# Kernel tuning notes

Measured on AMD Instinct MI355X. Metric: run time of the kernel, lower is better.

Reference implementation:

```python
import jax, jax.numpy as jnp
import numpy as np

B, S, D, H = 2, 2048, 1024, 16
DK = D // H


def setup_inputs() -> dict:
    key = jax.random.key(0)
    ks = jax.random.split(key, 8)
    Q = jax.random.normal(ks[0], (B, S, D), dtype=jnp.float32)
    K = jax.random.normal(ks[1], (B, S, D), dtype=jnp.float32)
    V = jax.random.normal(ks[2], (B, S, D), dtype=jnp.float32)
    scale = 0.02
    W_q = jax.random.normal(ks[3], (D, D), dtype=jnp.float32) * scale
    W_k = jax.random.normal(ks[4], (D, D), dtype=jnp.float32) * scale
    W_v = jax.random.normal(ks[5], (D, D), dtype=jnp.float32) * scale
    W_o = jax.random.normal(ks[6], (D, D), dtype=jnp.float32) * scale
    b_q = jnp.zeros((D,), jnp.float32)
    b_k = jnp.zeros((D,), jnp.float32)
    b_v = jnp.zeros((D,), jnp.float32)
    b_o = jnp.zeros((D,), jnp.float32)
    # causal mask, broadcastable [1,1,S,S]; mask==0 positions are masked out
    mask = jnp.tril(jnp.ones((S, S), jnp.int32))[None, None, :, :]
    return dict(Q=Q, K=K, V=V, W_q=W_q, b_q=b_q, W_k=W_k, b_k=b_k,
                W_v=W_v, b_v=b_v, W_o=W_o, b_o=b_o, mask=mask)


def reference(Q, K, V, W_q, b_q, W_k, b_k, W_v, b_v, W_o, b_o, mask):
    # linear projections (torch Linear equivalent up to weight layout)
    q = Q @ W_q + b_q   # [B,S,D]
    k = K @ W_k + b_k
    v = V @ W_v + b_v
    # split heads -> [B,H,S,DK]
    q = q.reshape(B, S, H, DK).transpose(0, 2, 1, 3)
    k = k.reshape(B, S, H, DK).transpose(0, 2, 1, 3)
    v = v.reshape(B, S, H, DK).transpose(0, 2, 1, 3)
    # scaled dot-product attention with explicit [B,H,S,S] scores
    scores = jnp.einsum('bhqd,bhkd->bhqk', q, k) / jnp.sqrt(jnp.float32(DK))
    scores = jnp.where(mask == 0, jnp.float32(-1e9), scores)
    attn = jax.nn.softmax(scores, axis=-1)
    out = jnp.einsum('bhqk,bhkd->bhqd', attn, v)
    # merge heads and output projection
    out = out.transpose(0, 2, 1, 3).reshape(B, S, D)
    return out @ W_o + b_o
```

## Files before the change

### kernel.cpp

```cpp
#include <hip/hip_runtime.h>


typedef unsigned short u16;
typedef __attribute__((ext_vector_type(8))) short s8v;
typedef __attribute__((ext_vector_type(4))) float f4v;

#define S_ 2048
#define D_ 1024
#define H_ 16
#define DK_ 64

__device__ __forceinline__ u16 f2bf(float f) {
  unsigned u = __builtin_bit_cast(unsigned, f);
  u += 0x7fffu + ((u >> 16) & 1u);
  return (u16)(u >> 16);
}
__device__ __forceinline__ u16 f2bf_t(float f) {
  return (u16)(__builtin_bit_cast(unsigned, f) >> 16);
}

__device__ __forceinline__ void gld_lds16(const u16* g, u16* l) {
  __builtin_amdgcn_global_load_lds(
      (const __attribute__((address_space(1))) unsigned int*)g,
      (__attribute__((address_space(3))) unsigned int*)l, 16, 0, 0);
}

__global__ __launch_bounds__(256) void prep(
    const float* __restrict__ Q, const float* __restrict__ K, const float* __restrict__ V,
    u16* __restrict__ Qc, u16* __restrict__ Kc, u16* __restrict__ Vc,
    const float* __restrict__ W0, const float* __restrict__ W1,
    const float* __restrict__ W2, const float* __restrict__ W3,
    u16* __restrict__ T0, u16* __restrict__ T1, u16* __restrict__ T2, u16* __restrict__ T3) {
  int bid = blockIdx.x, tid = threadIdx.x;
  if (bid < 3072) {
    int z = bid >> 10, t = bid & 1023;
    const float* s = z == 0 ? Q : z == 1 ? K : V;
    u16*         d = z == 0 ? Qc : z == 1 ? Kc : Vc;
    const int n4 = (2 * S_ * D_) / 4;
    for (int idx = t * 256 + tid; idx < n4; idx += 1024 * 256) {
      float4 f = ((const float4*)s)[idx];
      unsigned lo = (unsigned)f2bf(f.x) | ((unsigned)f2bf(f.y) << 16);
      unsigned hi = (unsigned)f2bf(f.z) | ((unsigned)f2bf(f.w) << 16);
      ((uint2*)d)[idx] = make_uint2(lo, hi);
    }
  } else {
    int wb = bid - 3072;
    int z = wb >> 10, t = wb & 1023;
    const float* W = z == 0 ? W0 : z == 1 ? W1 : z == 2 ? W2 : W3;
    u16*         T = z == 0 ? T0 : z == 1 ? T1 : z == 2 ? T2 : T3;
    __shared__ float tile[32][33];
    int tx = tid & 31, ty = tid >> 5;
    int c0 = (t & 31) * 32, r0 = (t >> 5) * 32;
#pragma unroll
    for (int i = 0; i < 32; i += 8)
      tile[ty + i][tx] = W[(size_t)(r0 + ty + i) * D_ + c0 + tx];
    __syncthreads();
#pragma unroll
    for (int i = 0; i < 32; i += 8)
      T[(size_t)(c0 + ty + i) * D_ + r0 + tx] = f2bf(tile[tx][ty + i]);
  }
}

#define BM_ 128
#define BK_ 64

template <int NJ, int MODE>
__device__ __forceinline__ void gemm_core(const u16* __restrict__ A, const u16* __restrict__ Bt,
                                          const float* __restrict__ bias, void* __restrict__ out,
                                          float oscale, u16* lds) {
  constexpr int BN = NJ * 32;
  u16* Al = lds;
  u16* Bl = lds + BM_ * BK_;
  int tid = threadIdx.x;
  int w = tid >> 6, lane = tid & 63, quad = lane >> 4, col = lane & 15;
  int wm = (w >> 1) * 64, wn = (w & 1) * (NJ * 16);
  int m0 = blockIdx.y * BM_, n0 = blockIdx.x * BN;
  f4v acc[4][NJ] = {};
  const u16* Ag = A + (size_t)m0 * 1024;
  const u16* Bg = Bt + (size_t)n0 * 1024;
  int sr = tid >> 3, ss = tid & 7;

  for (int k0 = 0; k0 < 1024; k0 += BK_) {
    __syncthreads();
#pragma unroll
    for (int c = 0; c < 4; ++c) {
      int r = c * 32 + sr;
      int gs = ss ^ (r & 7);
      gld_lds16(Ag + (size_t)r * 1024 + k0 + gs * 8, &Al[r * BK_ + ss * 8]);
    }
#pragma unroll
    for (int c = 0; c < BN / 32; ++c) {
      int r = c * 32 + sr;
      int gs = ss ^ (r & 7);
      gld_lds16(Bg + (size_t)r * 1024 + k0 + gs * 8, &Bl[r * BK_ + ss * 8]);
    }
    __syncthreads();
#pragma unroll
    for (int hf = 0; hf < 2; ++hf) {
      s8v af[4], bfr[NJ];
#pragma unroll
      for (int i = 0; i < 4; ++i) {
        int row = wm + i * 16 + col;
        int sl = (hf * 4 + quad) ^ (row & 7);
        af[i] = *(const s8v*)&Al[row * BK_ + sl * 8];
      }
#pragma unroll
      for (int j = 0; j < NJ; ++j) {
        int row = wn + j * 16 + col;
        int sl = (hf * 4 + quad) ^ (row & 7);
        bfr[j] = *(const s8v*)&Bl[row * BK_ + sl * 8];
      }
#pragma unroll
      for (int i = 0; i < 4; ++i)
#pragma unroll
        for (int j = 0; j < NJ; ++j)
          acc[i][j] = __builtin_amdgcn_mfma_f32_16x16x32_bf16(af[i], bfr[j], acc[i][j], 0, 0, 0);
    }
  }

  if (MODE == 1) {
    __syncthreads();
    u16* scr = lds + w * 2304;
    int h = (n0 + wn) >> 6;
    int dkl = lane & 31, sh = (lane >> 5) * 32;
    int mg0 = m0 + wm + sh;
    int bb = mg0 >> 11, s0g = mg0 & 2047;
    u16* ob = (u16*)out + ((size_t)(bb * H_ + h) * DK_) * S_;
#pragma unroll
    for (int t = 0; t < 2; ++t) {
#pragma unroll
      for (int j2 = 2 * t; j2 < 2 * t + 2; ++j2) {
        float bv = bias[n0 + wn + j2 * 16 + col];
        int rloc = j2 * 16 + col - t * 32;
#pragma unroll
        for (int i = 0; i < 4; ++i)
#pragma unroll
          for (int r = 0; r < 4; ++r)
            scr[rloc * 72 + i * 16 + quad * 4 + r] = f2bf(acc[i][j2][r] + bv);
      }
      __builtin_amdgcn_wave_barrier();
      u16* op = ob + (size_t)(t * 32 + dkl) * S_ + s0g;
#pragma unroll
      for (int c = 0; c < 4; ++c)
        *(uint4*)&op[c * 8] = *(const uint4*)&scr[dkl * 72 + sh + c * 8];
      __builtin_amdgcn_wave_barrier();
    }
    return;
  }

#pragma unroll
  for (int i = 0; i < 4; ++i) {
#pragma unroll
    for (int j = 0; j < NJ; ++j) {
      int n = n0 + wn + j * 16 + col;
      float bb = bias[n];
#pragma unroll
      for (int r = 0; r < 4; ++r) {
        int m = m0 + wm + i * 16 + quad * 4 + r;
        float v = (acc[i][j][r] + bb) * oscale;
        if (MODE == 2) {
          ((float*)out)[(size_t)m * 1024 + n] = v;
        } else {
          int b = m >> 11, s = m & 2047, h = n >> 6, dk = n & 63;
          ((u16*)out)[((size_t)(b * H_ + h) * S_ + s) * DK_ + dk] = f2bf(v);
        }
      }
    }
  }
}

#define CEXPQ 0.18033688f

__global__ __launch_bounds__(256) void gemm_qkv(
    const u16* __restrict__ A0, const u16* __restrict__ A1, const u16* __restrict__ A2,
    const u16* __restrict__ B0, const u16* __restrict__ B1, const u16* __restrict__ B2,
    const float* __restrict__ bi0, const float* __restrict__ bi1, const float* __restrict__ bi2,
    u16* __restrict__ o0, u16* __restrict__ o1, u16* __restrict__ o2) {
  __shared__ __attribute__((aligned(16))) u16 lds[BM_ * BK_ + 128 * BK_];
  int z = blockIdx.z;
  const u16* A = z == 0 ? A0 : z == 1 ? A1 : A2;
  const u16* Bt = z == 0 ? B0 : z == 1 ? B1 : B2;
  const float* bias = z == 0 ? bi0 : z == 1 ? bi1 : bi2;
  u16* o = z == 0 ? o0 : z == 1 ? o1 : o2;
  if (z == 2)
    gemm_core<4, 1>(A, Bt, bias, o, 1.0f, lds);
  else
    gemm_core<4, 0>(A, Bt, bias, o, z == 0 ? CEXPQ : 1.0f, lds);
}

__global__ __launch_bounds__(256, 5) void gemm_out(const u16* __restrict__ A, const u16* __restrict__ Bt,
                                                   const float* __restrict__ bias, float* __restrict__ out) {
  __shared__ __attribute__((aligned(16))) u16 lds[BM_ * BK_ + 64 * BK_];
  gemm_core<2, 2>(A, Bt, bias, out, 1.0f, lds);
}

#define KT_ 64
#define PSTR 72

__global__ __launch_bounds__(256) void attn_fused(const u16* __restrict__ qb, const u16* __restrict__ kb,
                                                  const u16* __restrict__ vtb, u16* __restrict__ ao) {
  __shared__ __attribute__((aligned(16))) u16 Kt[KT_ * PSTR];
  __shared__ __attribute__((aligned(16))) u16 Vts[DK_ * PSTR];
  __shared__ __attribute__((aligned(16))) u16 Pl[4][16 * PSTR];
  int bh = blockIdx.y, b = bh >> 4, h = bh & 15;
  int j = blockIdx.x;
  int lo_base = j * 64, hi_base = (31 - j) * 64;
  int tid = threadIdx.x, w = tid >> 6, lane = tid & 63, quad = lane >> 4, col = lane & 15;
  const u16* Qh = qb + (size_t)bh * S_ * DK_;
  const u16* Kh = kb + (size_t)bh * S_ * DK_;
  const u16* Vh = vtb + (size_t)bh * DK_ * S_;
  int krow = tid >> 3, kcol = (tid & 7) * 8;

  int lo_qmin = lo_base + w * 16, hi_qmin = hi_base + w * 16;
  s8v qlo0 = *(const s8v*)(Qh + (size_t)(lo_qmin + col) * DK_ + quad * 8);
  s8v qlo1 = *(const s8v*)(Qh + (size_t)(lo_qmin + col) * DK_ + 32 + quad * 8);
  s8v qhi0 = *(const s8v*)(Qh + (size_t)(hi_qmin + col) * DK_ + quad * 8);
  s8v qhi1 = *(const s8v*)(Qh + (size_t)(hi_qmin + col) * DK_ + 32 + quad * 8);

  f4v Olo[4] = {}, Ohi[4] = {};
  float lslo[4] = {}, lshi[4] = {};

  int nk = hi_base + 64;
  uint4 k0r = *(const uint4*)(Kh + (size_t)krow * DK_ + kcol);
  uint4 k1r = *(const uint4*)(Kh + (size_t)(32 + krow) * DK_ + kcol);
  uint4 v0r = *(const uint4*)(Vh + (size_t)krow * S_ + kcol);
  uint4 v1r = *(const uint4*)(Vh + (size_t)(32 + krow) * S_ + kcol);

  for (int kt = 0; kt < nk; kt += KT_) {
    __syncthreads();
    *(uint4*)&Kt[krow * PSTR + kcol] = k0r;
    *(uint4*)&Kt[(32 + krow) * PSTR + kcol] = k1r;
    *(uint4*)&Vts[krow * PSTR + kcol] = v0r;
    *(uint4*)&Vts[(32 + krow) * PSTR + kcol] = v1r;
    __syncthreads();
    int kn = kt + KT_;
    if (kn < nk) {
      k0r = *(const uint4*)(Kh + (size_t)(kn + krow) * DK_ + kcol);
      k1r = *(const uint4*)(Kh + (size_t)(kn + 32 + krow) * DK_ + kcol);
      v0r = *(const uint4*)(Vh + (size_t)krow * S_ + kn + kcol);
      v1r = *(const uint4*)(Vh + (size_t)(32 + krow) * S_ + kn + kcol);
    }

    s8v kf[4][2], vf[4][2];
#pragma unroll
    for (int ks = 0; ks < 4; ++ks) {
      kf[ks][0] = *(const s8v*)&Kt[(ks * 16 + col) * PSTR + quad * 8];
      kf[ks][1] = *(const s8v*)&Kt[(ks * 16 + col) * PSTR + 32 + quad * 8];
    }
#pragma unroll
    for (int d = 0; d < 4; ++d) {
      vf[d][0] = *(const s8v*)&Vts[(d * 16 + col) * PSTR + quad * 8];
      vf[d][1] = *(const s8v*)&Vts[(d * 16 + col) * PSTR + 32 + quad * 8];
    }

    auto process = [&](const s8v& q0, const s8v& q1, int qmin, f4v* O, float* ls) {
      f4v sc[4];
#pragma unroll
      for (int ks = 0; ks < 4; ++ks) {
        f4v t = {0.f, 0.f, 0.f, 0.f};
        t = __builtin_amdgcn_mfma_f32_16x16x32_bf16(q0, kf[ks][0], t, 0, 0, 0);
        t = __builtin_amdgcn_mfma_f32_16x16x32_bf16(q1, kf[ks][1], t, 0, 0, 0);
        sc[ks] = t;
      }
      bool full = (kt + KT_ - 1 <= qmin);
#pragma unroll
      for (int r = 0; r < 4; ++r) {
        float p0, p1, p2, p3;
        if (full) {
          p0 = exp2f(sc[0][r]);
          p1 = exp2f(sc[1][r]);
          p2 = exp2f(sc[2][r]);
          p3 = exp2f(sc[3][r]);
        } else {
          int qr = qmin + quad * 4 + r;
          p0 = (kt + col)      <= qr ? exp2f(sc[0][r]) : 0.f;
          p1 = (kt + 16 + col) <= qr ? exp2f(sc[1][r]) : 0.f;
          p2 = (kt + 32 + col) <= qr ? exp2f(sc[2][r]) : 0.f;
          p3 = (kt + 48 + col) <= qr ? exp2f(sc[3][r]) : 0.f;
        }
        ls[r] += (p0 + p1) + (p2 + p3);
        int row = quad * 4 + r;
        Pl[w][row * PSTR + col]      = f2bf_t(p0);
        Pl[w][row * PSTR + 16 + col] = f2bf_t(p1);
        Pl[w][row * PSTR + 32 + col] = f2bf_t(p2);
        Pl[w][row * PSTR + 48 + col] = f2bf_t(p3);
      }
      __builtin_amdgcn_wave_barrier();
      s8v pa0 = *(const s8v*)&Pl[w][col * PSTR + quad * 8];
      s8v pa1 = *(const s8v*)&Pl[w][col * PSTR + 32 + quad * 8];
#pragma unroll
      for (int d = 0; d < 4; ++d) {
        O[d] = __builtin_amdgcn_mfma_f32_16x16x32_bf16(pa0, vf[d][0], O[d], 0, 0, 0);
        O[d] = __builtin_amdgcn_mfma_f32_16x16x32_bf16(pa1, vf[d][1], O[d], 0, 0, 0);
      }
      __builtin_amdgcn_wave_barrier();
    };

    process(qhi0, qhi1, hi_qmin, Ohi, lshi);
    if (kt <= lo_qmin + 15)
      process(qlo0, qlo1, lo_qmin, Olo, lslo);
  }

#pragma unroll
  for (int g = 0; g < 2; ++g) {
    f4v* O = g ? Olo : Ohi;
    float* ls = g ? lslo : lshi;
    int qmin = g ? lo_qmin : hi_qmin;
#pragma unroll
    for (int r = 0; r < 4; ++r) {
      float l = ls[r];
      l += __shfl_xor(l, 1);
      l += __shfl_xor(l, 2);
      l += __shfl_xor(l, 4);
      l += __shfl_xor(l, 8);
      float inv = 1.0f / l;
      size_t row = (size_t)(b * S_ + qmin + quad * 4 + r);
#pragma unroll
      for (int d = 0; d < 4; ++d)
        ao[row * D_ + h * DK_ + d * 16 + col] = f2bf(O[d][r] * inv);
    }
  }
}

extern "C" void kernel_launch(void* const* d_in, const int* in_sizes, int n_in,
                              void* d_out, int out_size, void* d_ws, size_t ws_size,
                              hipStream_t stream) {
  const float* Q  = (const float*)d_in[0];
  const float* K  = (const float*)d_in[1];
  const float* V  = (const float*)d_in[2];
  const float* Wq = (const float*)d_in[3];
  const float* bq = (const float*)d_in[4];
  const float* Wk = (const float*)d_in[5];
  const float* bk = (const float*)d_in[6];
  const float* Wv = (const float*)d_in[7];
  const float* bv = (const float*)d_in[8];
  const float* Wo = (const float*)d_in[9];
  const float* bo = (const float*)d_in[10];

  char* p = (char*)d_ws;
  const size_t TEN = (size_t)2 * S_ * D_ * 2;
  const size_t WT  = (size_t)D_ * D_ * 2;
  u16* Qc  = (u16*)p; p += TEN;
  u16* Kc  = (u16*)p; p += TEN;
  u16* Vc  = (u16*)p; p += TEN;
  u16* Wqt = (u16*)p; p += WT;
  u16* Wkt = (u16*)p; p += WT;
  u16* Wvt = (u16*)p; p += WT;
  u16* Wot = (u16*)p; p += WT;
  u16* qb  = (u16*)p; p += TEN;
  u16* kbf = (u16*)p; p += TEN;
  u16* vtb = (u16*)p; p += TEN;
  u16* ao  = (u16*)p; p += TEN;

  prep<<<7168, 256, 0, stream>>>(Q, K, V, Qc, Kc, Vc, Wq, Wk, Wv, Wo, Wqt, Wkt, Wvt, Wot);
  gemm_qkv<<<dim3(D_ / 128, 32, 3), 256, 0, stream>>>(Qc, Kc, Vc, Wqt, Wkt, Wvt, bq, bk, bv, qb, kbf, vtb);
  attn_fused<<<dim3(16, 2 * H_), 256, 0, stream>>>(qb, kbf, vtb, ao);
  gemm_out<<<dim3(D_ / 64, 32), 256, 0, stream>>>(ao, Wot, bo, (float*)d_out);
}
```

Before: 243.4 us.

## Split attention hi/lo query tiles across 8 waves and shrink output GEMM tile

The attention kernel moves from 256 threads, where each wave handles both a high and a low query tile, to 512 threads where waves 0-3 take the high tile and waves 4-7 the low tile. K/V staging is spread over all threads, and low-tile waves skip compute once past their causal range. This doubles the waves per block to raise latency hiding and parallelism over a 512-block grid. The output GEMM is templated to a 64x64 tile with a doubled grid so more blocks are available. The cost is load imbalance between the two wave groups and more per-block tile overhead in the smaller GEMM.

```diff
diff --git a/kernel.cpp b/kernel.cpp
--- a/kernel.cpp
+++ b/kernel.cpp
@@ -61,21 +61,21 @@
   }
 }
 
-#define BM_ 128
 #define BK_ 64
 
-template <int NJ, int MODE>
+template <int MI, int NJ, int MODE>
 __device__ __forceinline__ void gemm_core(const u16* __restrict__ A, const u16* __restrict__ Bt,
                                           const float* __restrict__ bias, void* __restrict__ out,
                                           float oscale, u16* lds) {
+  constexpr int BM = MI * 32;
   constexpr int BN = NJ * 32;
   u16* Al = lds;
-  u16* Bl = lds + BM_ * BK_;
+  u16* Bl = lds + BM * BK_;
   int tid = threadIdx.x;
   int w = tid >> 6, lane = tid & 63, quad = lane >> 4, col = lane & 15;
-  int wm = (w >> 1) * 64, wn = (w & 1) * (NJ * 16);
-  int m0 = blockIdx.y * BM_, n0 = blockIdx.x * BN;
-  f4v acc[4][NJ] = {};
+  int wm = (w >> 1) * (MI * 16), wn = (w & 1) * (NJ * 16);
+  int m0 = blockIdx.y * BM, n0 = blockIdx.x * BN;
+  f4v acc[MI][NJ] = {};
   const u16* Ag = A + (size_t)m0 * 1024;
   const u16* Bg = Bt + (size_t)n0 * 1024;
   int sr = tid >> 3, ss = tid & 7;
@@ -83,7 +83,7 @@
   for (int k0 = 0; k0 < 1024; k0 += BK_) {
     __syncthreads();
 #pragma unroll
-    for (int c = 0; c < 4; ++c) {
+    for (int c = 0; c < BM / 32; ++c) {
       int r = c * 32 + sr;
       int gs = ss ^ (r & 7);
       gld_lds16(Ag + (size_t)r * 1024 + k0 + gs * 8, &Al[r * BK_ + ss * 8]);
@@ -97,9 +97,9 @@
     __syncthreads();
 #pragma unroll
     for (int hf = 0; hf < 2; ++hf) {
-      s8v af[4], bfr[NJ];
-#pragma unroll
-      for (int i = 0; i < 4; ++i) {
+      s8v af[MI], bfr[NJ];
+#pragma unroll
+      for (int i = 0; i < MI; ++i) {
         int row = wm + i * 16 + col;
         int sl = (hf * 4 + quad) ^ (row & 7);
         af[i] = *(const s8v*)&Al[row * BK_ + sl * 8];
@@ -111,7 +111,7 @@
         bfr[j] = *(const s8v*)&Bl[row * BK_ + sl * 8];
       }
 #pragma unroll
-      for (int i = 0; i < 4; ++i)
+      for (int i = 0; i < MI; ++i)
 #pragma unroll
         for (int j = 0; j < NJ; ++j)
           acc[i][j] = __builtin_amdgcn_mfma_f32_16x16x32_bf16(af[i], bfr[j], acc[i][j], 0, 0, 0);
@@ -133,7 +133,7 @@
         float bv = bias[n0 + wn + j2 * 16 + col];
         int rloc = j2 * 16 + col - t * 32;
 #pragma unroll
-        for (int i = 0; i < 4; ++i)
+        for (int i = 0; i < MI; ++i)
 #pragma unroll
           for (int r = 0; r < 4; ++r)
             scr[rloc * 72 + i * 16 + quad * 4 + r] = f2bf(acc[i][j2][r] + bv);
@@ -149,7 +149,7 @@
   }
 
 #pragma unroll
-  for (int i = 0; i < 4; ++i) {
+  for (int i = 0; i < MI; ++i) {
 #pragma unroll
     for (int j = 0; j < NJ; ++j) {
       int n = n0 + wn + j * 16 + col;
@@ -176,149 +176,132 @@
     const u16* __restrict__ B0, const u16* __restrict__ B1, const u16* __restrict__ B2,
     const float* __restrict__ bi0, const float* __restrict__ bi1, const float* __restrict__ bi2,
     u16* __restrict__ o0, u16* __restrict__ o1, u16* __restrict__ o2) {
-  __shared__ __attribute__((aligned(16))) u16 lds[BM_ * BK_ + 128 * BK_];
+  __shared__ __attribute__((aligned(16))) u16 lds[128 * BK_ + 128 * BK_];
   int z = blockIdx.z;
   const u16* A = z == 0 ? A0 : z == 1 ? A1 : A2;
   const u16* Bt = z == 0 ? B0 : z == 1 ? B1 : B2;
   const float* bias = z == 0 ? bi0 : z == 1 ? bi1 : bi2;
   u16* o = z == 0 ? o0 : z == 1 ? o1 : o2;
   if (z == 2)
-    gemm_core<4, 1>(A, Bt, bias, o, 1.0f, lds);
+    gemm_core<4, 4, 1>(A, Bt, bias, o, 1.0f, lds);
   else
-    gemm_core<4, 0>(A, Bt, bias, o, z == 0 ? CEXPQ : 1.0f, lds);
-}
-
-__global__ __launch_bounds__(256, 5) void gemm_out(const u16* __restrict__ A, const u16* __restrict__ Bt,
+    gemm_core<4, 4, 0>(A, Bt, bias, o, z == 0 ? CEXPQ : 1.0f, lds);
+}
+
+__global__ __launch_bounds__(256, 4) void gemm_out(const u16* __restrict__ A, const u16* __restrict__ Bt,
                                                    const float* __restrict__ bias, float* __restrict__ out) {
-  __shared__ __attribute__((aligned(16))) u16 lds[BM_ * BK_ + 64 * BK_];
-  gemm_core<2, 2>(A, Bt, bias, out, 1.0f, lds);
+  __shared__ __attribute__((aligned(16))) u16 lds[64 * BK_ + 64 * BK_];
+  gemm_core<2, 2, 2>(A, Bt, bias, out, 1.0f, lds);
 }
 
 #define KT_ 64
 #define PSTR 72
 
-__global__ __launch_bounds__(256) void attn_fused(const u16* __restrict__ qb, const u16* __restrict__ kb,
-                                                  const u16* __restrict__ vtb, u16* __restrict__ ao) {
+__global__ __launch_bounds__(512, 4) void attn_fused(const u16* __restrict__ qb, const u16* __restrict__ kb,
+                                                     const u16* __restrict__ vtb, u16* __restrict__ ao) {
   __shared__ __attribute__((aligned(16))) u16 Kt[KT_ * PSTR];
   __shared__ __attribute__((aligned(16))) u16 Vts[DK_ * PSTR];
-  __shared__ __attribute__((aligned(16))) u16 Pl[4][16 * PSTR];
+  __shared__ __attribute__((aligned(16))) u16 Pl[8][16 * PSTR];
   int bh = blockIdx.y, b = bh >> 4, h = bh & 15;
   int j = blockIdx.x;
-  int lo_base = j * 64, hi_base = (31 - j) * 64;
   int tid = threadIdx.x, w = tid >> 6, lane = tid & 63, quad = lane >> 4, col = lane & 15;
+  int sub = w & 3;
+  int base = (w < 4) ? (31 - j) * 64 : j * 64;
+  int qmin = base + sub * 16;
+  int nk = (32 - j) * 64;
+
   const u16* Qh = qb + (size_t)bh * S_ * DK_;
   const u16* Kh = kb + (size_t)bh * S_ * DK_;
   const u16* Vh = vtb + (size_t)bh * DK_ * S_;
-  int krow = tid >> 3, kcol = (tid & 7) * 8;
-
-  int lo_qmin = lo_base + w * 16, hi_qmin = hi_base + w * 16;
-  s8v qlo0 = *(const s8v*)(Qh + (size_t)(lo_qmin + col) * DK_ + quad * 8);
-  s8v qlo1 = *(const s8v*)(Qh + (size_t)(lo_qmin + col) * DK_ + 32 + quad * 8);
-  s8v qhi0 = *(const s8v*)(Qh + (size_t)(hi_qmin + col) * DK_ + quad * 8);
-  s8v qhi1 = *(const s8v*)(Qh + (size_t)(hi_qmin + col) * DK_ + 32 + quad * 8);
-
-  f4v Olo[4] = {}, Ohi[4] = {};
-  float lslo[4] = {}, lshi[4] = {};
-
-  int nk = hi_base + 64;
-  uint4 k0r = *(const uint4*)(Kh + (size_t)krow * DK_ + kcol);
-  uint4 k1r = *(const uint4*)(Kh + (size_t)(32 + krow) * DK_ + kcol);
-  uint4 v0r = *(const uint4*)(Vh + (size_t)krow * S_ + kcol);
-  uint4 v1r = *(const uint4*)(Vh + (size_t)(32 + krow) * S_ + kcol);
+
+  s8v qf0 = *(const s8v*)(Qh + (size_t)(qmin + col) * DK_ + quad * 8);
+  s8v qf1 = *(const s8v*)(Qh + (size_t)(qmin + col) * DK_ + 32 + quad * 8);
+
+  f4v O[4] = {};
+  float ls[4] = {};
+
+  int st = tid & 255;
+  bool stK = tid < 256;
+  int srow = st >> 2, soff = (st & 3) * 16;
+  u16* sl = stK ? &Kt[srow * PSTR + soff] : &Vts[srow * PSTR + soff];
+  const u16* g0 = stK ? Kh + (size_t)srow * DK_ + soff : Vh + (size_t)srow * S_ + soff;
+  uint4 preA = *(const uint4*)g0;
+  uint4 preB = *(const uint4*)(g0 + 8);
 
   for (int kt = 0; kt < nk; kt += KT_) {
     __syncthreads();
-    *(uint4*)&Kt[krow * PSTR + kcol] = k0r;
-    *(uint4*)&Kt[(32 + krow) * PSTR + kcol] = k1r;
-    *(uint4*)&Vts[krow * PSTR + kcol] = v0r;
-    *(uint4*)&Vts[(32 + krow) * PSTR + kcol] = v1r;
+    *(uint4*)sl = preA;
+    *(uint4*)(sl + 8) = preB;
     __syncthreads();
     int kn = kt + KT_;
     if (kn < nk) {
-      k0r = *(const uint4*)(Kh + (size_t)(kn + krow) * DK_ + kcol);
-      k1r = *(const uint4*)(Kh + (size_t)(kn + 32 + krow) * DK_ + kcol);
-      v0r = *(const uint4*)(Vh + (size_t)krow * S_ + kn + kcol);
-      v1r = *(const uint4*)(Vh + (size_t)(32 + krow) * S_ + kn + kcol);
-    }
-
-    s8v kf[4][2], vf[4][2];
+      const u16* gn = stK ? Kh + (size_t)(kn + srow) * DK_ + soff
+                          : Vh + (size_t)srow * S_ + kn + soff;
+      preA = *(const uint4*)gn;
+      preB = *(const uint4*)(gn + 8);
+    }
+    if (kt > qmin + 15) continue;
+
+    f4v sc[4];
 #pragma unroll
     for (int ks = 0; ks < 4; ++ks) {
-      kf[ks][0] = *(const s8v*)&Kt[(ks * 16 + col) * PSTR + quad * 8];
-      kf[ks][1] = *(const s8v*)&Kt[(ks * 16 + col) * PSTR + 32 + quad * 8];
-    }
+      s8v kf0 = *(const s8v*)&Kt[(ks * 16 + col) * PSTR + quad * 8];
+      s8v kf1 = *(const s8v*)&Kt[(ks * 16 + col) * PSTR + 32 + quad * 8];
+      f4v t = {0.f, 0.f, 0.f, 0.f};
+      t = __builtin_amdgcn_mfma_f32_16x16x32_bf16(qf0, kf0, t, 0, 0, 0);
+      t = __builtin_amdgcn_mfma_f32_16x16x32_bf16(qf1, kf1, t, 0, 0, 0);
+      sc[ks] = t;
+    }
+
+    bool full = (kt + KT_ - 1 <= qmin);
+#pragma unroll
+    for (int r = 0; r < 4; ++r) {
+      float p0, p1, p2, p3;
+      if (full) {
+        p0 = exp2f(sc[0][r]);
+        p1 = exp2f(sc[1][r]);
+        p2 = exp2f(sc[2][r]);
+        p3 = exp2f(sc[3][r]);
+      } else {
+        int qr = qmin + quad * 4 + r;
+        p0 = (kt + col)      <= qr ? exp2f(sc[0][r]) : 0.f;
+        p1 = (kt + 16 + col) <= qr ? exp2f(sc[1][r]) : 0.f;
+        p2 = (kt + 32 + col) <= qr ? exp2f(sc[2][r]) : 0.f;
+        p3 = (kt + 48 + col) <= qr ? exp2f(sc[3][r]) : 0.f;
+      }
+      ls[r] += (p0 + p1) + (p2 + p3);
+      int row = quad * 4 + r;
+      Pl[w][row * PSTR + col]      = f2bf_t(p0);
+      Pl[w][row * PSTR + 16 + col] = f2bf_t(p1);
+      Pl[w][row * PSTR + 32 + col] = f2bf_t(p2);
+      Pl[w][row * PSTR + 48 + col] = f2bf_t(p3);
+    }
+    __builtin_amdgcn_wave_barrier();
+
+    s8v pa0 = *(const s8v*)&Pl[w][col * PSTR + quad * 8];
+    s8v pa1 = *(const s8v*)&Pl[w][col * PSTR + 32 + quad * 8];
 #pragma unroll
     for (int d = 0; d < 4; ++d) {
-      vf[d][0] = *(const s8v*)&Vts[(d * 16 + col) * PSTR + quad * 8];
-      vf[d][1] = *(const s8v*)&Vts[(d * 16 + col) * PSTR + 32 + quad * 8];
-    }
-
-    auto process = [&](const s8v& q0, const s8v& q1, int qmin, f4v* O, float* ls) {
-      f4v sc[4];
-#pragma unroll
-      for (int ks = 0; ks < 4; ++ks) {
-        f4v t = {0.f, 0.f, 0.f, 0.f};
-        t = __builtin_amdgcn_mfma_f32_16x16x32_bf16(q0, kf[ks][0], t, 0, 0, 0);
-        t = __builtin_amdgcn_mfma_f32_16x16x32_bf16(q1, kf[ks][1], t, 0, 0, 0);
-        sc[ks] = t;
-      }
-      bool full = (kt + KT_ - 1 <= qmin);
-#pragma unroll
-      for (int r = 0; r < 4; ++r) {
-        float p0, p1, p2, p3;
-        if (full) {
-          p0 = exp2f(sc[0][r]);
-          p1 = exp2f(sc[1][r]);
-          p2 = exp2f(sc[2][r]);
-          p3 = exp2f(sc[3][r]);
-        } else {
-          int qr = qmin + quad * 4 + r;
-          p0 = (kt + col)      <= qr ? exp2f(sc[0][r]) : 0.f;
-          p1 = (kt + 16 + col) <= qr ? exp2f(sc[1][r]) : 0.f;
-          p2 = (kt + 32 + col) <= qr ? exp2f(sc[2][r]) : 0.f;
-          p3 = (kt + 48 + col) <= qr ? exp2f(sc[3][r]) : 0.f;
-        }
-        ls[r] += (p0 + p1) + (p2 + p3);
-        int row = quad * 4 + r;
-        Pl[w][row * PSTR + col]      = f2bf_t(p0);
-        Pl[w][row * PSTR + 16 + col] = f2bf_t(p1);
-        Pl[w][row * PSTR + 32 + col] = f2bf_t(p2);
-        Pl[w][row * PSTR + 48 + col] = f2bf_t(p3);
-      }
-      __builtin_amdgcn_wave_barrier();
-      s8v pa0 = *(const s8v*)&Pl[w][col * PSTR + quad * 8];
-      s8v pa1 = *(const s8v*)&Pl[w][col * PSTR + 32 + quad * 8];
-#pragma unroll
-      for (int d = 0; d < 4; ++d) {
-        O[d] = __builtin_amdgcn_mfma_f32_16x16x32_bf16(pa0, vf[d][0], O[d], 0, 0, 0);
-        O[d] = __builtin_amdgcn_mfma_f32_16x16x32_bf16(pa1, vf[d][1], O[d], 0, 0, 0);
-      }
-      __builtin_amdgcn_wave_barrier();
-    };
-
-    process(qhi0, qhi1, hi_qmin, Ohi, lshi);
-    if (kt <= lo_qmin + 15)
-      process(qlo0, qlo1, lo_qmin, Olo, lslo);
-  }
-
-#pragma unroll
-  for (int g = 0; g < 2; ++g) {
-    f4v* O = g ? Olo : Ohi;
-    float* ls = g ? lslo : lshi;
-    int qmin = g ? lo_qmin : hi_qmin;
-#pragma unroll
-    for (int r = 0; r < 4; ++r) {
-      float l = ls[r];
-      l += __shfl_xor(l, 1);
-      l += __shfl_xor(l, 2);
-      l += __shfl_xor(l, 4);
-      l += __shfl_xor(l, 8);
-      float inv = 1.0f / l;
-      size_t row = (size_t)(b * S_ + qmin + quad * 4 + r);
-#pragma unroll
-      for (int d = 0; d < 4; ++d)
-        ao[row * D_ + h * DK_ + d * 16 + col] = f2bf(O[d][r] * inv);
-    }
+      s8v vf0 = *(const s8v*)&Vts[(d * 16 + col) * PSTR + quad * 8];
+      s8v vf1 = *(const s8v*)&Vts[(d * 16 + col) * PSTR + 32 + quad * 8];
+      O[d] = __builtin_amdgcn_mfma_f32_16x16x32_bf16(pa0, vf0, O[d], 0, 0, 0);
+      O[d] = __builtin_amdgcn_mfma_f32_16x16x32_bf16(pa1, vf1, O[d], 0, 0, 0);
+    }
+    __builtin_amdgcn_wave_barrier();
+  }
+
+#pragma unroll
+  for (int r = 0; r < 4; ++r) {
+    float l = ls[r];
+    l += __shfl_xor(l, 1);
+    l += __shfl_xor(l, 2);
+    l += __shfl_xor(l, 4);
+    l += __shfl_xor(l, 8);
+    float inv = 1.0f / l;
+    size_t row = (size_t)(b * S_ + qmin + quad * 4 + r);
+#pragma unroll
+    for (int d = 0; d < 4; ++d)
+      ao[row * D_ + h * DK_ + d * 16 + col] = f2bf(O[d][r] * inv);
   }
 }
 
@@ -354,6 +337,6 @@
 
   prep<<<7168, 256, 0, stream>>>(Q, K, V, Qc, Kc, Vc, Wq, Wk, Wv, Wo, Wqt, Wkt, Wvt, Wot);
   gemm_qkv<<<dim3(D_ / 128, 32, 3), 256, 0, stream>>>(Qc, Kc, Vc, Wqt, Wkt, Wvt, bq, bk, bv, qb, kbf, vtb);
-  attn_fused<<<dim3(16, 2 * H_), 256, 0, stream>>>(qb, kbf, vtb, ao);
-  gemm_out<<<dim3(D_ / 64, 32), 256, 0, stream>>>(ao, Wot, bo, (float*)d_out);
-}
+  attn_fused<<<dim3(16, 2 * H_), 512, 0, stream>>>(qb, kbf, vtb, ao);
+  gemm_out<<<dim3(D_ / 64, 64), 256, 0, stream>>>(ao, Wot, bo, (float*)d_out);
+}
```

After: 235.7 us. -3.2%, faster.
